# Performance work log

Hardware: AMD Instinct MI355X
Metric: run time of the kernel (lower is better)

The kernel has to match this reference:

```python
import jax, jax.numpy as jnp
import numpy as np

DIM = 1024
HEADS = 16
DHEAD = 64
INNER = HEADS * DHEAD
B, N = 1, 2048
ROPE_BASE = 10000.0
LN_EPS = 1e-5


def rope_tables(seq_len, d, dtype):
    # theta_i = 1 / base^(2i/d); emb = cat(freqs, freqs) -> cos/sin [N, d]
    theta = 1.0 / (ROPE_BASE ** (jnp.arange(0, d, 2, dtype=dtype) / d))
    pos = jnp.arange(seq_len, dtype=dtype)
    freqs = pos[:, None] * theta[None, :]          # [N, d/2]
    emb = jnp.concatenate([freqs, freqs], axis=-1)  # [N, d]
    return jnp.cos(emb), jnp.sin(emb)


def apply_rotary(x, cos, sin):
    # x: [B,H,N,D], cos/sin: [N,D]; interleaved rotation as in the torch code
    x1, x2 = x[..., ::2], x[..., 1::2]
    x_rot = jnp.stack([-x2, x1], axis=-1).reshape(x.shape)
    return x * cos + x_rot * sin


def setup_inputs() -> dict:
    key = jax.random.key(0)
    ks = jax.random.split(key, 6)
    x = jax.random.normal(ks[0], (B, N, DIM), dtype=jnp.float32)
    gamma = jnp.ones((DIM,), dtype=jnp.float32)
    Wq = jax.random.normal(ks[1], (DIM, INNER), dtype=jnp.float32) * 0.02
    Wkv = jax.random.normal(ks[2], (DIM, 2 * INNER), dtype=jnp.float32) * 0.02
    # near-identity per-head bilinear transform (torch inits toward identity)
    W_bilinear = jnp.eye(DHEAD, dtype=jnp.float32)[None] + \
        jax.random.normal(ks[3], (HEADS, DHEAD, DHEAD), dtype=jnp.float32) * 0.02
    Wo = jax.random.normal(ks[4], (INNER, DIM), dtype=jnp.float32) * 0.02
    return {"x": x, "gamma": gamma, "Wq": Wq, "Wkv": Wkv,
            "W_bilinear": W_bilinear, "Wo": Wo}


def reference(x, gamma, Wq, Wkv, W_bilinear, Wo):
    b, n, _ = x.shape
    # LayerNorm (beta = 0 buffer)
    mu = jnp.mean(x, axis=-1, keepdims=True)
    var = jnp.var(x, axis=-1, keepdims=True)
    xn = (x - mu) / jnp.sqrt(var + LN_EPS) * gamma

    q = xn @ Wq                                    # [B,N,INNER]
    kv = xn @ Wkv                                  # [B,N,2*INNER]
    k, v = jnp.split(kv, 2, axis=-1)

    def to_heads(t):
        return t.reshape(b, n, HEADS, DHEAD).transpose(0, 2, 1, 3)  # [B,H,N,D]

    q, k, v = map(to_heads, (q, k, v))

    cos, sin = rope_tables(n, DHEAD, x.dtype)
    q = apply_rotary(q, cos, sin) * (DHEAD ** -0.5)
    k = apply_rotary(k, cos, sin)

    # per-head bilinear transform of K
    kt = jnp.einsum('bhnd,hde->bhne', k, W_bilinear)
    sim = jnp.einsum('bhid,bhjd->bhij', q, kt)      # [B,H,N,N]
    attn = jax.nn.softmax(sim, axis=-1)
    out = jnp.einsum('bhij,bhjd->bhid', attn, v)    # [B,H,N,D]
    out = out.transpose(0, 2, 1, 3).reshape(b, n, INNER)
    return out @ Wo
```

## Files before the change

### kernel.cpp

```cpp
#include <hip/hip_runtime.h>


typedef unsigned short u16;
typedef __attribute__((ext_vector_type(4))) float f32x4;
typedef __attribute__((ext_vector_type(8))) __bf16 bf16x8;

struct alignas(8) US4 { u16 x, y, z, w; };

__device__ __forceinline__ u16 f2bf(float f) {
  union { float f; unsigned u; } v; v.f = f;
  unsigned r = v.u + 0x7FFFu + ((v.u >> 16) & 1u);
  return (u16)(r >> 16);
}

typedef void GVOID __attribute__((address_space(1)));
typedef void LVOID __attribute__((address_space(3)));

#if defined(__has_builtin)
#if __has_builtin(__builtin_amdgcn_global_load_lds)
#define HAS_GLD_LDS 1
#endif
#endif

__device__ __forceinline__ void gld16(const void* g, void* l) {
#ifdef HAS_GLD_LDS
  __builtin_amdgcn_global_load_lds((GVOID*)(void*)g, (LVOID*)l, 16, 0, 0);
#else
  struct alignas(16) U4 { unsigned a, b, c, d; };
  *(U4*)l = *(const U4*)g;
#endif
}

__device__ __forceinline__ f32x4 MFMA(bf16x8 a, bf16x8 b, f32x4 c) {
  return __builtin_amdgcn_mfma_f32_16x16x32_bf16(a, b, c, 0, 0, 0);
}

__device__ __forceinline__ int swz(int r, int q) {
  return r * 32 + ((q ^ ((r >> 1) & 3)) << 3);
}
__device__ __forceinline__ int swz_src_colb(int o) {
  const int r = o >> 6;
  return ((((o >> 4) & 3) ^ ((r >> 1) & 3)) << 4);
}

__global__ __launch_bounds__(256) void prep_kernel(
    const float* __restrict__ x, const float* __restrict__ gamma,
    const float* __restrict__ Wq, const float* __restrict__ Wkv,
    const float* __restrict__ Wo, const float* __restrict__ Wb,
    u16* __restrict__ xn, u16* __restrict__ wqkvT, u16* __restrict__ woT,
    u16* __restrict__ wbT) {
  __shared__ __align__(16) float smem[32 * 33];
  const int bid = blockIdx.x, t = threadIdx.x;
  if (bid < 4160) {
    const float* src; u16* dst; int C, R, bx, by;
    if (bid < 1024)      { src = Wq;  dst = wqkvT;              R = 1024; C = 1024; bx = bid & 31; by = bid >> 5; }
    else if (bid < 3072) { int i = bid - 1024; src = Wkv; dst = wqkvT + 1024 * 1024; R = 1024; C = 2048; bx = i & 63; by = i >> 6; }
    else if (bid < 4096) { int i = bid - 3072; src = Wo;  dst = woT; R = 1024; C = 1024; bx = i & 31; by = i >> 5; }
    else { int i = bid - 4096; int h = i >> 2; src = Wb + (size_t)h * 4096; dst = wbT + (size_t)h * 4096; R = 64; C = 64; bx = i & 1; by = (i >> 1) & 1; }
    float (*tile)[33] = (float(*)[33])smem;
    const int c0 = bx * 32, r0 = by * 32;
    const int tx = t & 31, ty = t >> 5;
#pragma unroll
    for (int i = 0; i < 4; i++)
      tile[ty + i * 8][tx] = src[(size_t)(r0 + ty + i * 8) * C + c0 + tx];
    __syncthreads();
#pragma unroll
    for (int i = 0; i < 4; i++)
      dst[(size_t)(c0 + ty + i * 8) * R + r0 + tx] = f2bf(tile[tx][ty + i * 8]);
  } else {
    const int n = bid - 4160;
    const int w = t >> 6, lane = t & 63;
    const float4 v = *(const float4*)&x[(size_t)n * 1024 + t * 4];
    float s = v.x + v.y + v.z + v.w;
    float q = v.x * v.x + v.y * v.y + v.z * v.z + v.w * v.w;
#pragma unroll
    for (int off = 32; off; off >>= 1) {
      s += __shfl_down(s, off);
      q += __shfl_down(q, off);
    }
    if (lane == 0) { smem[w] = s; smem[4 + w] = q; }
    __syncthreads();
    s = smem[0] + smem[1] + smem[2] + smem[3];
    q = smem[4] + smem[5] + smem[6] + smem[7];
    const float mean = s * (1.0f / 1024.0f);
    const float var = q * (1.0f / 1024.0f) - mean * mean;
    const float inv = rsqrtf(var + 1e-5f);
    const float4 g = *(const float4*)&gamma[t * 4];
    US4 o;
    o.x = f2bf((v.x - mean) * inv * g.x);
    o.y = f2bf((v.y - mean) * inv * g.y);
    o.z = f2bf((v.z - mean) * inv * g.z);
    o.w = f2bf((v.w - mean) * inv * g.w);
    *(US4*)&xn[(size_t)n * 1024 + t * 4] = o;
  }
}

__global__ __launch_bounds__(256, 2) void gemm_qkv(
    const u16* __restrict__ A, const u16* __restrict__ B,
    u16* __restrict__ qh, u16* __restrict__ kr, u16* __restrict__ vh) {
  __shared__ u16 As[128 * 32];
  __shared__ u16 Bs[128 * 32];
  const int K = 1024;
  const int t = threadIdx.x;
  const int w = t >> 6, lane = t & 63, quad = lane >> 4, cc = lane & 15;
  const int bm = blockIdx.y << 7, bn = blockIdx.x << 7;
  const int wm = (w >> 1) << 6, wn = (w & 1) << 6;
  const f32x4 fzero = {0.f, 0.f, 0.f, 0.f};
  f32x4 acc[4][4];
#pragma unroll
  for (int i = 0; i < 4; i++)
#pragma unroll
    for (int j = 0; j < 4; j++) acc[i][j] = fzero;

  const char* gA = (const char*)A;
  const char* gB = (const char*)B;
  for (int k0 = 0; k0 < K; k0 += 32) {
    __syncthreads();
#pragma unroll
    for (int i = 0; i < 2; i++) {
      const int o = (i * 256 + t) * 16;
      const int row = o >> 6, colb = swz_src_colb(o);
      gld16(gA + (((size_t)(bm + row) * K + k0) << 1) + colb, (char*)As + o);
      gld16(gB + (((size_t)(bn + row) * K + k0) << 1) + colb, (char*)Bs + o);
    }
    __syncthreads();
    bf16x8 af[4], bfr[4];
#pragma unroll
    for (int mi = 0; mi < 4; mi++)
      af[mi] = *(const bf16x8*)&As[swz(wm + mi * 16 + cc, quad)];
#pragma unroll
    for (int ni = 0; ni < 4; ni++)
      bfr[ni] = *(const bf16x8*)&Bs[swz(wn + ni * 16 + cc, quad)];
#pragma unroll
    for (int mi = 0; mi < 4; mi++)
#pragma unroll
      for (int ni = 0; ni < 4; ni++)
        acc[mi][ni] = MFMA(af[mi], bfr[ni], acc[mi][ni]);
  }

  const int region = blockIdx.x >> 3;
  if (region == 2) {
#pragma unroll
    for (int ni = 0; ni < 4; ni++) {
      const int col = bn + wn + ni * 16 + cc;
      const int h = (col >> 6) & 15, d = col & 63;
#pragma unroll
      for (int mi = 0; mi < 4; mi++) {
        const int row0 = bm + wm + mi * 16 + quad * 4;
#pragma unroll
        for (int r = 0; r < 4; r++)
          vh[((size_t)h * 2048 + row0 + r) * 64 + d] = f2bf(acc[mi][ni][r]);
      }
    }
  } else {
    const float sc = (region == 0) ? 0.125f : 1.0f;
    u16* dst = (region == 0) ? qh : kr;
#pragma unroll
    for (int ni = 0; ni < 4; ni++) {
      const int col = bn + wn + ni * 16 + cc;
      const int h = (col >> 6) & 15, d = col & 63;
      const float theta = __expf(-(float)(col & 31) * 0.2878231366242557f);
      const float sgn = (col & 1) ? 1.0f : -1.0f;
#pragma unroll
      for (int mi = 0; mi < 4; mi++) {
        const int row0 = bm + wm + mi * 16 + quad * 4;
#pragma unroll
        for (int r = 0; r < 4; r++) {
          const float val = acc[mi][ni][r];
          const float part = __shfl_xor(val, 1);
          float sv, cv;
          __sincosf(theta * (float)(row0 + r), &sv, &cv);
          dst[((size_t)h * 2048 + row0 + r) * 64 + d] =
              f2bf((val * cv + sgn * part * sv) * sc);
        }
      }
    }
  }
}

__global__ __launch_bounds__(256, 2) void mid_kernel(
    const u16* __restrict__ kr, const u16* __restrict__ wbT,
    u16* __restrict__ kth, const u16* __restrict__ vh, u16* __restrict__ vt) {
  __shared__ __align__(16) u16 smem[4224];
  const int bid = blockIdx.x, t = threadIdx.x;
  if (bid < 512) {
    const int h = bid >> 5, bm = (bid & 31) << 6;
    u16* As = smem;
    u16* Bs = smem + 2048;
    const int w = t >> 6, lane = t & 63, quad = lane >> 4, cc = lane & 15;
    const int wm = (w >> 1) << 5, wn = (w & 1) << 5;
    const f32x4 fzero = {0.f, 0.f, 0.f, 0.f};
    f32x4 acc[2][2];
#pragma unroll
    for (int i = 0; i < 2; i++)
#pragma unroll
      for (int j = 0; j < 2; j++) acc[i][j] = fzero;
    const char* gA = (const char*)(kr + (size_t)h * 2048 * 64);
    const char* gB = (const char*)(wbT + (size_t)h * 4096);
#pragma unroll
    for (int k0 = 0; k0 < 64; k0 += 32) {
      __syncthreads();
      {
        const int o = t * 16;
        const int row = o >> 6, colb = swz_src_colb(o);
        gld16(gA + (((size_t)(bm + row) * 64 + k0) << 1) + colb, (char*)As + o);
        gld16(gB + (((size_t)row * 64 + k0) << 1) + colb, (char*)Bs + o);
      }
      __syncthreads();
      bf16x8 af[2], bfr[2];
#pragma unroll
      for (int mi = 0; mi < 2; mi++)
        af[mi] = *(const bf16x8*)&As[swz(wm + mi * 16 + cc, quad)];
#pragma unroll
      for (int ni = 0; ni < 2; ni++)
        bfr[ni] = *(const bf16x8*)&Bs[swz(wn + ni * 16 + cc, quad)];
#pragma unroll
      for (int mi = 0; mi < 2; mi++)
#pragma unroll
        for (int ni = 0; ni < 2; ni++)
          acc[mi][ni] = MFMA(af[mi], bfr[ni], acc[mi][ni]);
    }
    u16* C = kth + (size_t)h * 2048 * 64;
#pragma unroll
    for (int mi = 0; mi < 2; mi++) {
      const int row = bm + wm + mi * 16 + quad * 4;
#pragma unroll
      for (int ni = 0; ni < 2; ni++) {
        const int col = wn + ni * 16 + cc;
#pragma unroll
        for (int r = 0; r < 4; r++)
          C[(size_t)(row + r) * 64 + col] = f2bf(acc[mi][ni][r]);
      }
    }
  } else {
    const int idx = bid - 512;
    const int h = idx >> 5, j0 = (idx & 31) * 64;
    u16 (*tile)[65] = (u16(*)[65])smem;
    const int tx = t & 63, ty = t >> 6;
    const u16* src = vh + ((size_t)h * 2048 + j0) * 64;
#pragma unroll
    for (int i = 0; i < 16; i++) tile[ty + i * 4][tx] = src[(ty + i * 4) * 64 + tx];
    __syncthreads();
    u16* dst = vt + (size_t)h * 64 * 2048 + j0;
#pragma unroll
    for (int i = 0; i < 16; i++)
      dst[(size_t)(ty + i * 4) * 2048 + tx] = tile[tx][ty + i * 4];
  }
}

__global__ __launch_bounds__(256, 2) void attn_kernel(
    const u16* __restrict__ qh, const u16* __restrict__ kth,
    const u16* __restrict__ vt, u16* __restrict__ aout) {
  __shared__ u16 Ks[2 * 128 * 32];
  __shared__ u16 Vs[4 * 64 * 32];
  __shared__ u16 Ps[4 * 64 * 56];
  const int t = threadIdx.x;
  const int w = t >> 6, lane = t & 63, quad = lane >> 4, cc = lane & 15;
  const int bid = blockIdx.x;
  const int h = (bid & 7) + ((bid >> 8) << 3);
  const int q0 = ((bid >> 3) & 31) << 6;
  const size_t hq = (size_t)h * (2048 * 64);
  const f32x4 fzero = {0.f, 0.f, 0.f, 0.f};

  bf16x8 ones;
  {
    union { u16 u; __bf16 b; } one; one.u = 0x3F80;
#pragma unroll
    for (int i = 0; i < 8; i++) ones[i] = one.b;
  }

#pragma unroll
  for (int i = 0; i < 2; i++) {
    const int o = (i * 256 + t) * 16;
    const int sub = o >> 12, row = (o >> 6) & 63, colb = swz_src_colb(o);
    gld16((const char*)qh + ((hq + (size_t)(q0 + row) * 64 + sub * 32) << 1) + colb,
          (char*)Ks + o);
  }
  __syncthreads();
  bf16x8 qf[4][2];
#pragma unroll
  for (int qn = 0; qn < 4; qn++)
#pragma unroll
    for (int ds = 0; ds < 2; ds++)
      qf[qn][ds] = *(const bf16x8*)&Ks[swz(ds * 64 + qn * 16 + cc, quad)];

  f32x4 oacc[4][4];
  f32x4 lacc[4];
#pragma unroll
  for (int mi = 0; mi < 4; mi++) {
    lacc[mi] = fzero;
#pragma unroll
    for (int et = 0; et < 4; et++) oacc[mi][et] = fzero;
  }

  for (int jt = 0; jt < 16; jt++) {
    const int j0 = jt << 7;
    __syncthreads();
#pragma unroll
    for (int i = 0; i < 4; i++) {
      const int o = (i * 256 + t) * 16;
      const int colb = swz_src_colb(o);
      const int sub = o >> 13, row = (o >> 6) & 127;
      gld16((const char*)kth + ((hq + (size_t)(j0 + row) * 64 + sub * 32) << 1) + colb,
            (char*)Ks + o);
      const int vsub = o >> 12, vrow = (o >> 6) & 63;
      gld16((const char*)vt + ((hq + (size_t)vrow * 2048 + j0 + vsub * 32) << 1) + colb,
            (char*)Vs + o);
    }
    __syncthreads();

#pragma unroll
    for (int jm = 0; jm < 2; jm++) {
      const bf16x8 kf0 = *(const bf16x8*)&Ks[swz(w * 32 + jm * 16 + cc, quad)];
      const bf16x8 kf1 = *(const bf16x8*)&Ks[swz(128 + w * 32 + jm * 16 + cc, quad)];
#pragma unroll
      for (int qn = 0; qn < 4; qn++) {
        f32x4 s = MFMA(kf0, qf[qn][0], fzero);
        s = MFMA(kf1, qf[qn][1], s);
        uint2 pk;
        pk.x = (unsigned)f2bf(__expf(s[0])) | ((unsigned)f2bf(__expf(s[1])) << 16);
        pk.y = (unsigned)f2bf(__expf(s[2])) | ((unsigned)f2bf(__expf(s[3])) << 16);
        *(uint2*)&Ps[(w * 64 + qn * 16 + cc) * 56 + jm * 16 + quad * 4] = pk;
      }
    }

    bf16x8 vf[4];
#pragma unroll
    for (int et = 0; et < 4; et++)
      vf[et] = *(const bf16x8*)&Vs[swz(w * 64 + et * 16 + cc, quad)];
#pragma unroll
    for (int mi = 0; mi < 4; mi++) {
      const bf16x8 pa = *(const bf16x8*)&Ps[(w * 64 + mi * 16 + cc) * 56 + quad * 8];
      lacc[mi] = MFMA(pa, ones, lacc[mi]);
#pragma unroll
      for (int et = 0; et < 4; et++) oacc[mi][et] = MFMA(pa, vf[et], oacc[mi][et]);
    }
  }

  float* OA = (float*)Ks;
  float* OB = (float*)Vs;
  float* lP = (float*)Ps;
  __syncthreads();
  if (w >= 2) {
    float* dst = (w == 2) ? OA : OB;
#pragma unroll
    for (int mi = 0; mi < 4; mi++) {
#pragma unroll
      for (int et = 0; et < 4; et++)
        *(f32x4*)&dst[(et * 16 + cc) * 64 + mi * 16 + quad * 4] = oacc[mi][et];
      if (cc == 0)
#pragma unroll
        for (int r = 0; r < 4; r++)
          lP[64 * w + mi * 16 + quad * 4 + r] = lacc[mi][r];
    }
  }
  __syncthreads();
  if (w < 2) {
    const float* src = (w == 0) ? OA : OB;
    const float* lsrc = &lP[64 * (w + 2)];
#pragma unroll
    for (int mi = 0; mi < 4; mi++) {
#pragma unroll
      for (int et = 0; et < 4; et++)
        oacc[mi][et] += *(const f32x4*)&src[(et * 16 + cc) * 64 + mi * 16 + quad * 4];
#pragma unroll
      for (int r = 0; r < 4; r++)
        lacc[mi][r] += lsrc[mi * 16 + quad * 4 + r];
    }
  }
  __syncthreads();
  if (w < 2) {
    float* dst = (w == 0) ? OA : OB;
#pragma unroll
    for (int mi = 0; mi < 4; mi++) {
#pragma unroll
      for (int et = 0; et < 4; et++)
        *(f32x4*)&dst[(et * 16 + cc) * 64 + mi * 16 + quad * 4] = oacc[mi][et];
      if (cc == 0)
#pragma unroll
        for (int r = 0; r < 4; r++)
          lP[64 * w + mi * 16 + quad * 4 + r] = lacc[mi][r];
    }
  }
  __syncthreads();
  {
    const int q = lane;
    const float linv = 1.0f / (lP[q] + lP[64 + q]);
    u16 obuf[16];
#pragma unroll
    for (int e = 0; e < 16; e++) {
      const int ee = w * 16 + e;
      obuf[e] = f2bf((OA[ee * 64 + q] + OB[ee * 64 + q]) * linv);
    }
    uint4* dst = (uint4*)&aout[(size_t)(q0 + q) * 1024 + h * 64 + w * 16];
    dst[0] = *(uint4*)&obuf[0];
    dst[1] = *(uint4*)&obuf[8];
  }
}

__global__ __launch_bounds__(256, 2) void gemm64_bt_f32(
    const u16* __restrict__ A, const u16* __restrict__ B, float* __restrict__ C,
    int M, int N, int K) {
  __shared__ u16 As[64 * 32];
  __shared__ u16 Bs[64 * 32];
  const int t = threadIdx.x;
  const int w = t >> 6, lane = t & 63, quad = lane >> 4, cc = lane & 15;
  const int bm = blockIdx.y << 6, bn = blockIdx.x << 6;
  const int wm = (w >> 1) << 5, wn = (w & 1) << 5;
  const f32x4 fzero = {0.f, 0.f, 0.f, 0.f};
  f32x4 acc[2][2];
#pragma unroll
  for (int i = 0; i < 2; i++)
#pragma unroll
    for (int j = 0; j < 2; j++) acc[i][j] = fzero;

  const char* gA = (const char*)A;
  const char* gB = (const char*)B;
  for (int k0 = 0; k0 < K; k0 += 32) {
    __syncthreads();
    {
      const int o = t * 16;
      const int row = o >> 6, colb = swz_src_colb(o);
      gld16(gA + (((size_t)(bm + row) * K + k0) << 1) + colb, (char*)As + o);
      gld16(gB + (((size_t)(bn + row) * K + k0) << 1) + colb, (char*)Bs + o);
    }
    __syncthreads();
    bf16x8 af[2], bfr[2];
#pragma unroll
    for (int mi = 0; mi < 2; mi++)
      af[mi] = *(const bf16x8*)&As[swz(wm + mi * 16 + cc, quad)];
#pragma unroll
    for (int ni = 0; ni < 2; ni++)
      bfr[ni] = *(const bf16x8*)&Bs[swz(wn + ni * 16 + cc, quad)];
#pragma unroll
    for (int mi = 0; mi < 2; mi++)
#pragma unroll
      for (int ni = 0; ni < 2; ni++)
        acc[mi][ni] = MFMA(af[mi], bfr[ni], acc[mi][ni]);
  }
#pragma unroll
  for (int mi = 0; mi < 2; mi++) {
    const int row = bm + wm + mi * 16 + quad * 4;
#pragma unroll
    for (int ni = 0; ni < 2; ni++) {
      const int col = bn + wn + ni * 16 + cc;
#pragma unroll
      for (int r = 0; r < 4; r++) C[(size_t)(row + r) * N + col] = acc[mi][ni][r];
    }
  }
}

extern "C" void kernel_launch(void* const* d_in, const int* in_sizes, int n_in,
                              void* d_out, int out_size, void* d_ws, size_t ws_size,
                              hipStream_t stream) {
  (void)in_sizes; (void)n_in; (void)out_size; (void)ws_size;
  const float* x     = (const float*)d_in[0];
  const float* gamma = (const float*)d_in[1];
  const float* Wq    = (const float*)d_in[2];
  const float* Wkv   = (const float*)d_in[3];
  const float* Wb    = (const float*)d_in[4];
  const float* Wo    = (const float*)d_in[5];
  float* out = (float*)d_out;
  char* ws = (char*)d_ws;

  const size_t OFF_XN    = 0;
  const size_t OFF_WQKVT = 4194304;
  const size_t OFF_WOT   = 10485760;
  const size_t OFF_WBT   = 12582912;
  const size_t OFF_QH    = 12713984;
  const size_t OFF_KR    = 16908288;
  const size_t OFF_KTH   = 21102592;
  const size_t OFF_VH    = 25296896;
  const size_t OFF_VT    = 29491200;
  const size_t OFF_AOUT  = 33685504;

  u16* xn    = (u16*)(ws + OFF_XN);
  u16* wqkvT = (u16*)(ws + OFF_WQKVT);
  u16* woT   = (u16*)(ws + OFF_WOT);
  u16* wbT   = (u16*)(ws + OFF_WBT);
  u16* qh    = (u16*)(ws + OFF_QH);
  u16* kr    = (u16*)(ws + OFF_KR);
  u16* kth   = (u16*)(ws + OFF_KTH);
  u16* vh    = (u16*)(ws + OFF_VH);
  u16* vt    = (u16*)(ws + OFF_VT);
  u16* aout  = (u16*)(ws + OFF_AOUT);

  prep_kernel<<<6208, 256, 0, stream>>>(x, gamma, Wq, Wkv, Wo, Wb,
                                        xn, wqkvT, woT, wbT);
  gemm_qkv<<<dim3(24, 16), 256, 0, stream>>>(xn, wqkvT, qh, kr, vh);
  mid_kernel<<<1024, 256, 0, stream>>>(kr, wbT, kth, vh, vt);
  attn_kernel<<<512, 256, 0, stream>>>(qh, kth, vt, aout);
  gemm64_bt_f32<<<dim3(16, 32), 256, 0, stream>>>(aout, woT, out, 2048, 1024, 1024);
}
```

Baseline: 159.7 us.

## Fuse K bilinear and V transpose into QKV GEMM, split attention over keys

Removes mid_kernel. The K-region blocks of the QKV GEMM now apply RoPE into shared memory and multiply by the per-head bilinear matrix in place. V is written directly in transposed layout. Attention is split into two halves over the key range (1024 blocks), and the partial O and l are combined through a global workspace with an atomic counter, where the second-arriving block finalizes. This cuts an intermediate round trip and a launch and raises parallelism, at the cost of extra fp32 partial traffic, a larger LDS footprint in gemm_qkv, and occupancy 3 for attention.

New measurement: 302.5 us. 1.89x slower.

```diff
diff --git a/kernel.cpp b/kernel.cpp
--- a/kernel.cpp
+++ b/kernel.cpp
@@ -48,9 +48,13 @@
     const float* __restrict__ Wq, const float* __restrict__ Wkv,
     const float* __restrict__ Wo, const float* __restrict__ Wb,
     u16* __restrict__ xn, u16* __restrict__ wqkvT, u16* __restrict__ woT,
-    u16* __restrict__ wbT) {
+    u16* __restrict__ wbT, int* __restrict__ cnt) {
   __shared__ __align__(16) float smem[32 * 33];
   const int bid = blockIdx.x, t = threadIdx.x;
+  if (bid == 0) {
+    uint2 z; z.x = 0; z.y = 0;
+    ((uint2*)cnt)[t] = z;
+  }
   if (bid < 4160) {
     const float* src; u16* dst; int C, R, bx, by;
     if (bid < 1024)      { src = Wq;  dst = wqkvT;              R = 1024; C = 1024; bx = bid & 31; by = bid >> 5; }
@@ -97,9 +101,11 @@
 
 __global__ __launch_bounds__(256, 2) void gemm_qkv(
     const u16* __restrict__ A, const u16* __restrict__ B,
-    u16* __restrict__ qh, u16* __restrict__ kr, u16* __restrict__ vh) {
+    const u16* __restrict__ wbT, u16* __restrict__ qh,
+    u16* __restrict__ kth, u16* __restrict__ vt) {
   __shared__ u16 As[128 * 32];
   __shared__ u16 Bs[128 * 32];
+  __shared__ u16 krs[2 * 8192];
   const int K = 1024;
   const int t = threadIdx.x;
   const int w = t >> 6, lane = t & 63, quad = lane >> 4, cc = lane & 15;
@@ -139,22 +145,7 @@
   }
 
   const int region = blockIdx.x >> 3;
-  if (region == 2) {
-#pragma unroll
-    for (int ni = 0; ni < 4; ni++) {
-      const int col = bn + wn + ni * 16 + cc;
-      const int h = (col >> 6) & 15, d = col & 63;
-#pragma unroll
-      for (int mi = 0; mi < 4; mi++) {
-        const int row0 = bm + wm + mi * 16 + quad * 4;
-#pragma unroll
-        for (int r = 0; r < 4; r++)
-          vh[((size_t)h * 2048 + row0 + r) * 64 + d] = f2bf(acc[mi][ni][r]);
-      }
-    }
-  } else {
-    const float sc = (region == 0) ? 0.125f : 1.0f;
-    u16* dst = (region == 0) ? qh : kr;
+  if (region == 0) {
 #pragma unroll
     for (int ni = 0; ni < 4; ni++) {
       const int col = bn + wn + ni * 16 + cc;
@@ -167,98 +158,122 @@
 #pragma unroll
         for (int r = 0; r < 4; r++) {
           const float val = acc[mi][ni][r];
-          const float part = __shfl_xor(val, 1);
+          const float pr = __shfl_xor(val, 1);
           float sv, cv;
           __sincosf(theta * (float)(row0 + r), &sv, &cv);
-          dst[((size_t)h * 2048 + row0 + r) * 64 + d] =
-              f2bf((val * cv + sgn * part * sv) * sc);
+          qh[((size_t)h * 2048 + row0 + r) * 64 + d] =
+              f2bf((val * cv + sgn * pr * sv) * 0.125f);
         }
       }
     }
-  }
-}
-
-__global__ __launch_bounds__(256, 2) void mid_kernel(
-    const u16* __restrict__ kr, const u16* __restrict__ wbT,
-    u16* __restrict__ kth, const u16* __restrict__ vh, u16* __restrict__ vt) {
-  __shared__ __align__(16) u16 smem[4224];
-  const int bid = blockIdx.x, t = threadIdx.x;
-  if (bid < 512) {
-    const int h = bid >> 5, bm = (bid & 31) << 6;
-    u16* As = smem;
-    u16* Bs = smem + 2048;
-    const int w = t >> 6, lane = t & 63, quad = lane >> 4, cc = lane & 15;
-    const int wm = (w >> 1) << 5, wn = (w & 1) << 5;
-    const f32x4 fzero = {0.f, 0.f, 0.f, 0.f};
-    f32x4 acc[2][2];
-#pragma unroll
-    for (int i = 0; i < 2; i++)
-#pragma unroll
-      for (int j = 0; j < 2; j++) acc[i][j] = fzero;
-    const char* gA = (const char*)(kr + (size_t)h * 2048 * 64);
-    const char* gB = (const char*)(wbT + (size_t)h * 4096);
-#pragma unroll
-    for (int k0 = 0; k0 < 64; k0 += 32) {
-      __syncthreads();
-      {
-        const int o = t * 16;
-        const int row = o >> 6, colb = swz_src_colb(o);
-        gld16(gA + (((size_t)(bm + row) * 64 + k0) << 1) + colb, (char*)As + o);
-        gld16(gB + (((size_t)row * 64 + k0) << 1) + colb, (char*)Bs + o);
+  } else if (region == 2) {
+#pragma unroll
+    for (int ni = 0; ni < 4; ni++) {
+      const int col = bn + wn + ni * 16 + cc;
+      const int h = (col >> 6) & 15, d = col & 63;
+      u16* base = vt + ((size_t)h * 64 + d) * 2048;
+#pragma unroll
+      for (int mi = 0; mi < 4; mi++) {
+        const int row0 = bm + wm + mi * 16 + quad * 4;
+        US4 pk;
+        pk.x = f2bf(acc[mi][ni][0]);
+        pk.y = f2bf(acc[mi][ni][1]);
+        pk.z = f2bf(acc[mi][ni][2]);
+        pk.w = f2bf(acc[mi][ni][3]);
+        *(US4*)&base[row0] = pk;
       }
-      __syncthreads();
-      bf16x8 af[2], bfr[2];
-#pragma unroll
-      for (int mi = 0; mi < 2; mi++)
-        af[mi] = *(const bf16x8*)&As[swz(wm + mi * 16 + cc, quad)];
-#pragma unroll
-      for (int ni = 0; ni < 2; ni++)
-        bfr[ni] = *(const bf16x8*)&Bs[swz(wn + ni * 16 + cc, quad)];
-#pragma unroll
-      for (int mi = 0; mi < 2; mi++)
-#pragma unroll
-        for (int ni = 0; ni < 2; ni++)
-          acc[mi][ni] = MFMA(af[mi], bfr[ni], acc[mi][ni]);
-    }
-    u16* C = kth + (size_t)h * 2048 * 64;
-#pragma unroll
-    for (int mi = 0; mi < 2; mi++) {
-      const int row = bm + wm + mi * 16 + quad * 4;
-#pragma unroll
-      for (int ni = 0; ni < 2; ni++) {
-        const int col = wn + ni * 16 + cc;
+    }
+  } else {
+    const int h2 = w & 1;
+    u16* krh = krs + h2 * 8192;
+#pragma unroll
+    for (int ni = 0; ni < 4; ni++) {
+      const int dloc = ni * 16 + cc;
+      const int dsub = dloc >> 5;
+      const int chunk = (dloc & 31) >> 3, elem = dloc & 7;
+      const int col = bn + wn + ni * 16 + cc;
+      const float theta = __expf(-(float)(col & 31) * 0.2878231366242557f);
+      const float sgn = (col & 1) ? 1.0f : -1.0f;
+#pragma unroll
+      for (int mi = 0; mi < 4; mi++) {
+        const int lrow0 = wm + mi * 16 + quad * 4;
+#pragma unroll
+        for (int r = 0; r < 4; r++) {
+          const float val = acc[mi][ni][r];
+          const float pr = __shfl_xor(val, 1);
+          float sv, cv;
+          __sincosf(theta * (float)(bm + lrow0 + r), &sv, &cv);
+          const int row = lrow0 + r;
+          krh[dsub * 4096 + row * 32 + ((chunk ^ ((row >> 1) & 3)) << 3) + elem] =
+              f2bf(val * cv + sgn * pr * sv);
+        }
+      }
+    }
+    __syncthreads();
+    const int hg0 = (bn >> 6) & 15;
+#pragma unroll
+    for (int i = 0; i < 2; i++) {
+      const int o = (i * 256 + t) * 16;
+      const int row = o >> 6;
+      const int dsub = row >> 6, e = row & 63;
+      const int colb = swz_src_colb(o);
+      gld16((const char*)wbT + (((size_t)hg0 * 4096 + e * 64 + dsub * 32) << 1) + colb,
+            (char*)As + o);
+      gld16((const char*)wbT + (((size_t)(hg0 + 1) * 4096 + e * 64 + dsub * 32) << 1) + colb,
+            (char*)Bs + o);
+    }
+    __syncthreads();
+    const int wmrow = (w >> 1) << 6;
+    const u16* Bsel = h2 ? Bs : As;
+    f32x4 acc2[4][4];
+#pragma unroll
+    for (int i = 0; i < 4; i++)
+#pragma unroll
+      for (int j = 0; j < 4; j++) acc2[i][j] = fzero;
+#pragma unroll
+    for (int dsub = 0; dsub < 2; dsub++) {
+      bf16x8 bfr[4];
+#pragma unroll
+      for (int et = 0; et < 4; et++)
+        bfr[et] = *(const bf16x8*)&Bsel[swz(dsub * 64 + et * 16 + cc, quad)];
+#pragma unroll
+      for (int mi = 0; mi < 4; mi++) {
+        const bf16x8 af = *(const bf16x8*)&krh[dsub * 4096 + swz(wmrow + mi * 16 + cc, quad)];
+#pragma unroll
+        for (int et = 0; et < 4; et++)
+          acc2[mi][et] = MFMA(af, bfr[et], acc2[mi][et]);
+      }
+    }
+    u16* Ck = kth + (size_t)(hg0 + h2) * 2048 * 64;
+#pragma unroll
+    for (int mi = 0; mi < 4; mi++) {
+      const int n0 = bm + wmrow + mi * 16 + quad * 4;
+#pragma unroll
+      for (int et = 0; et < 4; et++) {
+        const int e = et * 16 + cc;
 #pragma unroll
         for (int r = 0; r < 4; r++)
-          C[(size_t)(row + r) * 64 + col] = f2bf(acc[mi][ni][r]);
+          Ck[(size_t)(n0 + r) * 64 + e] = f2bf(acc2[mi][et][r]);
       }
     }
-  } else {
-    const int idx = bid - 512;
-    const int h = idx >> 5, j0 = (idx & 31) * 64;
-    u16 (*tile)[65] = (u16(*)[65])smem;
-    const int tx = t & 63, ty = t >> 6;
-    const u16* src = vh + ((size_t)h * 2048 + j0) * 64;
-#pragma unroll
-    for (int i = 0; i < 16; i++) tile[ty + i * 4][tx] = src[(ty + i * 4) * 64 + tx];
-    __syncthreads();
-    u16* dst = vt + (size_t)h * 64 * 2048 + j0;
-#pragma unroll
-    for (int i = 0; i < 16; i++)
-      dst[(size_t)(ty + i * 4) * 2048 + tx] = tile[tx][ty + i * 4];
-  }
-}
-
-__global__ __launch_bounds__(256, 2) void attn_kernel(
+  }
+}
+
+__global__ __launch_bounds__(256, 3) void attn_kernel(
     const u16* __restrict__ qh, const u16* __restrict__ kth,
-    const u16* __restrict__ vt, u16* __restrict__ aout) {
+    const u16* __restrict__ vt, u16* __restrict__ aout,
+    float* __restrict__ part, float* __restrict__ lpart, int* __restrict__ cnt) {
   __shared__ u16 Ks[2 * 128 * 32];
   __shared__ u16 Vs[4 * 64 * 32];
-  __shared__ u16 Ps[4 * 64 * 56];
+  __shared__ u16 Ps[4 * 64 * 40];
+  __shared__ int winflag;
   const int t = threadIdx.x;
   const int w = t >> 6, lane = t & 63, quad = lane >> 4, cc = lane & 15;
   const int bid = blockIdx.x;
-  const int h = (bid & 7) + ((bid >> 8) << 3);
-  const int q0 = ((bid >> 3) & 31) << 6;
+  const int h = bid & 15;
+  const int qt = (bid >> 4) & 31;
+  const int jh = bid >> 9;
+  const int q0 = qt << 6;
   const size_t hq = (size_t)h * (2048 * 64);
   const f32x4 fzero = {0.f, 0.f, 0.f, 0.f};
 
@@ -293,7 +308,7 @@
     for (int et = 0; et < 4; et++) oacc[mi][et] = fzero;
   }
 
-  for (int jt = 0; jt < 16; jt++) {
+  for (int jt = jh * 8; jt < jh * 8 + 8; jt++) {
     const int j0 = jt << 7;
     __syncthreads();
 #pragma unroll
@@ -320,7 +335,7 @@
         uint2 pk;
         pk.x = (unsigned)f2bf(__expf(s[0])) | ((unsigned)f2bf(__expf(s[1])) << 16);
         pk.y = (unsigned)f2bf(__expf(s[2])) | ((unsigned)f2bf(__expf(s[3])) << 16);
-        *(uint2*)&Ps[(w * 64 + qn * 16 + cc) * 56 + jm * 16 + quad * 4] = pk;
+        *(uint2*)&Ps[(w * 64 + qn * 16 + cc) * 40 + jm * 16 + quad * 4] = pk;
       }
     }
 
@@ -330,7 +345,7 @@
       vf[et] = *(const bf16x8*)&Vs[swz(w * 64 + et * 16 + cc, quad)];
 #pragma unroll
     for (int mi = 0; mi < 4; mi++) {
-      const bf16x8 pa = *(const bf16x8*)&Ps[(w * 64 + mi * 16 + cc) * 56 + quad * 8];
+      const bf16x8 pa = *(const bf16x8*)&Ps[(w * 64 + mi * 16 + cc) * 40 + quad * 8];
       lacc[mi] = MFMA(pa, ones, lacc[mi]);
 #pragma unroll
       for (int et = 0; et < 4; et++) oacc[mi][et] = MFMA(pa, vf[et], oacc[mi][et]);
@@ -383,14 +398,35 @@
     }
   }
   __syncthreads();
+
+  const int pairIdx = (qt << 4) | h;
+  float* myO = part + ((size_t)(pairIdx * 2 + jh) << 12);
+  float* myL = lpart + ((pairIdx * 2 + jh) << 6);
   {
     const int q = lane;
-    const float linv = 1.0f / (lP[q] + lP[64 + q]);
-    u16 obuf[16];
 #pragma unroll
     for (int e = 0; e < 16; e++) {
       const int ee = w * 16 + e;
-      obuf[e] = f2bf((OA[ee * 64 + q] + OB[ee * 64 + q]) * linv);
+      myO[ee * 64 + q] = OA[ee * 64 + q] + OB[ee * 64 + q];
+    }
+    if (t < 64) myL[t] = lP[t] + lP[64 + t];
+  }
+  __threadfence();
+  __syncthreads();
+  if (t == 0) winflag = (atomicAdd(&cnt[pairIdx], 1) == 1);
+  __syncthreads();
+  if (!winflag) return;
+  __threadfence();
+  const float* sO = part + ((size_t)(pairIdx * 2 + (1 - jh)) << 12);
+  const float* sL = lpart + ((pairIdx * 2 + (1 - jh)) << 6);
+  {
+    const int q = lane;
+    const float linv = 1.0f / (lP[q] + lP[64 + q] + sL[q]);
+    u16 obuf[16];
+#pragma unroll
+    for (int e = 0; e < 16; e++) {
+      const int ee = w * 16 + e;
+      obuf[e] = f2bf((OA[ee * 64 + q] + OB[ee * 64 + q] + sO[ee * 64 + q]) * linv);
     }
     uint4* dst = (uint4*)&aout[(size_t)(q0 + q) * 1024 + h * 64 + w * 16];
     dst[0] = *(uint4*)&obuf[0];
@@ -468,27 +504,28 @@
   const size_t OFF_WOT   = 10485760;
   const size_t OFF_WBT   = 12582912;
   const size_t OFF_QH    = 12713984;
-  const size_t OFF_KR    = 16908288;
-  const size_t OFF_KTH   = 21102592;
-  const size_t OFF_VH    = 25296896;
-  const size_t OFF_VT    = 29491200;
-  const size_t OFF_AOUT  = 33685504;
-
-  u16* xn    = (u16*)(ws + OFF_XN);
-  u16* wqkvT = (u16*)(ws + OFF_WQKVT);
-  u16* woT   = (u16*)(ws + OFF_WOT);
-  u16* wbT   = (u16*)(ws + OFF_WBT);
-  u16* qh    = (u16*)(ws + OFF_QH);
-  u16* kr    = (u16*)(ws + OFF_KR);
-  u16* kth   = (u16*)(ws + OFF_KTH);
-  u16* vh    = (u16*)(ws + OFF_VH);
-  u16* vt    = (u16*)(ws + OFF_VT);
-  u16* aout  = (u16*)(ws + OFF_AOUT);
+  const size_t OFF_KTH   = 16908288;
+  const size_t OFF_VT    = 21102592;
+  const size_t OFF_AOUT  = 25296896;
+  const size_t OFF_PART  = 29491200;
+  const size_t OFF_LPART = 46268416;
+  const size_t OFF_CNT   = 46530560;
+
+  u16*   xn    = (u16*)(ws + OFF_XN);
+  u16*   wqkvT = (u16*)(ws + OFF_WQKVT);
+  u16*   woT   = (u16*)(ws + OFF_WOT);
+  u16*   wbT   = (u16*)(ws + OFF_WBT);
+  u16*   qh    = (u16*)(ws + OFF_QH);
+  u16*   kth   = (u16*)(ws + OFF_KTH);
+  u16*   vt    = (u16*)(ws + OFF_VT);
+  u16*   aout  = (u16*)(ws + OFF_AOUT);
+  float* part  = (float*)(ws + OFF_PART);
+  float* lpart = (float*)(ws + OFF_LPART);
+  int*   cnt   = (int*)(ws + OFF_CNT);
 
   prep_kernel<<<6208, 256, 0, stream>>>(x, gamma, Wq, Wkv, Wo, Wb,
-                                        xn, wqkvT, woT, wbT);
-  gemm_qkv<<<dim3(24, 16), 256, 0, stream>>>(xn, wqkvT, qh, kr, vh);
-  mid_kernel<<<1024, 256, 0, stream>>>(kr, wbT, kth, vh, vt);
-  attn_kernel<<<512, 256, 0, stream>>>(qh, kth, vt, aout);
+                                        xn, wqkvT, woT, wbT, cnt);
+  gemm_qkv<<<dim3(24, 16), 256, 0, stream>>>(xn, wqkvT, wbT, qh, kth, vt);
+  attn_kernel<<<1024, 256, 0, stream>>>(qh, kth, vt, aout, part, lpart, cnt);
   gemm64_bt_f32<<<dim3(16, 32), 256, 0, stream>>>(aout, woT, out, 2048, 1024, 1024);
 }
```
